# Kernel tuning notes

Measured on AMD Instinct MI355X. Metric: run time of the kernel, lower is better.

Reference implementation:

```python
import jax, jax.numpy as jnp
import numpy as np

N_NODES = 131072
N_EDGES = 4194304
H1, H2 = 16, 1


def setup_inputs() -> dict:
    key = jax.random.key(0)
    k = jax.random.split(key, 6)
    x = jax.random.uniform(k[0], (N_NODES, 2), dtype=jnp.float32)
    edge_index = jax.random.randint(k[1], (2, N_EDGES), 0, N_NODES, dtype=jnp.int64)
    # GCNConv weights (glorot-ish scale) and zero biases
    W1 = jax.random.normal(k[2], (2, H1), dtype=jnp.float32) * 0.5
    b1 = jnp.zeros((H1,), dtype=jnp.float32)
    W2 = jax.random.normal(k[3], (H1, H2), dtype=jnp.float32) * 0.25
    b2 = jnp.zeros((H2,), dtype=jnp.float32)
    return {"x": x, "W1": W1, "b1": b1, "W2": W2, "b2": b2, "edge_index": edge_index}


def gcn_layer(x, W, b, src, dst, n):
    # PyG GCNConv: h = D^{-1/2} (A+I) D^{-1/2} (x W) + b  (self-loops already in src/dst)
    h = x @ W                                              # [N, F_out]
    deg = jax.ops.segment_sum(jnp.ones(dst.shape[0], h.dtype), dst, num_segments=n)
    dinv = jax.lax.rsqrt(deg)                              # deg >= 1 thanks to self-loops
    norm = dinv[src] * dinv[dst]                           # [E+N]
    out = jax.ops.segment_sum(h[src] * norm[:, None], dst, num_segments=n)
    return out + b


def reference(x, W1, b1, W2, b2, edge_index):
    n = x.shape[0]
    loops = jnp.arange(n, dtype=edge_index.dtype)
    src = jnp.concatenate([edge_index[0], loops])          # add self-loops once
    dst = jnp.concatenate([edge_index[1], loops])
    h = jax.nn.relu(gcn_layer(x, W1, b1, src, dst, n))
    h = gcn_layer(h, W2, b2, src, dst, n)                  # [N, 1]
    scores = jax.nn.sigmoid(h)
    return scores[edge_index[0]]                           # gather per-edge source score [E, 1]
```

## Files before the change

### kernel.cpp

```cpp
#include <hip/hip_runtime.h>
#include <cmath>

typedef unsigned int uint;
typedef unsigned short u16;

constexpr int N  = 131072;
constexpr int E  = 4194304;
constexpr int F  = 16;
constexpr int NB = 512;
constexpr int NBLK  = 512;
constexpr int SCT   = 512;
constexpr int CHUNK = 8192;
constexpr int EPT   = 16;
constexpr int CAPB  = 9216;
constexpr int LT    = 1024;

constexpr float S1 = 4194304.0f;
constexpr float S2 = 65536.0f;

__global__ void __launch_bounds__(SCT) k_scatter(
        const int* __restrict__ src, const int* __restrict__ dst,
        uint* __restrict__ part, u16* __restrict__ cnt16, u16* __restrict__ dir16) {
    __shared__ uint h[NB];
    __shared__ uint wsum[8];
    __shared__ uint vals[CHUNK];
    int t = threadIdx.x, g = blockIdx.x;
    int lane = t & 63, w = t >> 6;
    h[t] = 0;
    __syncthreads();
    int d[EPT], s[EPT];
    const int4* src4 = (const int4*)src;
    const int4* dst4 = (const int4*)dst;
    int base4 = g * (CHUNK / 4);
#pragma unroll
    for (int k = 0; k < EPT / 4; ++k) {
        int4 d4 = dst4[base4 + k * SCT + t];
        int4 s4 = src4[base4 + k * SCT + t];
        d[4 * k + 0] = d4.x; d[4 * k + 1] = d4.y; d[4 * k + 2] = d4.z; d[4 * k + 3] = d4.w;
        s[4 * k + 0] = s4.x; s[4 * k + 1] = s4.y; s[4 * k + 2] = s4.z; s[4 * k + 3] = s4.w;
        atomicAdd(&h[d4.x >> 8], 1u);
        atomicAdd(&h[d4.y >> 8], 1u);
        atomicAdd(&h[d4.z >> 8], 1u);
        atomicAdd(&h[d4.w >> 8], 1u);
    }
    __syncthreads();
    uint v = h[t];
    uint sv = v;
#pragma unroll
    for (int off = 1; off < 64; off <<= 1) {
        uint n = __shfl_up(sv, off);
        if (lane >= off) sv += n;
    }
    if (lane == 63) wsum[w] = sv;
    __syncthreads();
    uint wo = 0;
    for (int i = 0; i < w; ++i) wo += wsum[i];
    sv += wo;
    uint ex = sv - v;
    cnt16[(size_t)t * NBLK + g] = (u16)v;
    dir16[(size_t)t * NBLK + g] = (u16)ex;
    __syncthreads();
    h[t] = ex;
    __syncthreads();
#pragma unroll
    for (int k = 0; k < EPT; ++k) {
        int b = d[k] >> 8;
        uint slot = atomicAdd(&h[b], 1u);
        vals[slot] = ((uint)s[k] << 8) | (uint)(d[k] & 255);
    }
    __syncthreads();
    uint4* part4 = (uint4*)(part + (size_t)g * CHUNK);
    const uint4* vals4 = (const uint4*)vals;
#pragma unroll
    for (int k = 0; k < EPT / 4; ++k)
        part4[k * SCT + t] = vals4[k * SCT + t];
}

__global__ void __launch_bounds__(SCT) k_gather(
        const uint* __restrict__ part, const u16* __restrict__ cnt16,
        const u16* __restrict__ dir16, const float* __restrict__ x,
        uint* __restrict__ part2, uint* __restrict__ blen,
        float* __restrict__ dinv, float2* __restrict__ y) {
    __shared__ uint ps[NB + 1];
    __shared__ uint segoff[NB];
    __shared__ uint hw[8 * 256];
    __shared__ uint wsum[8];
    __shared__ uint stage[CAPB];
    int t = threadIdx.x, b = blockIdx.x;
    int lane = t & 63, w = t >> 6;
#pragma unroll
    for (int k = 0; k < 4; ++k) hw[k * SCT + t] = 0;
    uint len = cnt16[(size_t)b * NBLK + t];
    segoff[t] = (uint)t * CHUNK + dir16[(size_t)b * NBLK + t];
    uint sv = len;
#pragma unroll
    for (int off = 1; off < 64; off <<= 1) {
        uint n = __shfl_up(sv, off);
        if (lane >= off) sv += n;
    }
    if (lane == 63) wsum[w] = sv;
    __syncthreads();
    uint wo = 0;
    for (int i = 0; i < w; ++i) wo += wsum[i];
    ps[t] = sv + wo - len;
    uint L = 0;
#pragma unroll
    for (int i = 0; i < 8; ++i) L += wsum[i];
    if (t == 0) ps[NB] = L;
    __syncthreads();
    for (uint i = t; i < L; i += SCT) {
        uint lo = 0, hi = NB;
        while (hi - lo > 1) {
            uint mid = (lo + hi) >> 1;
            if (ps[mid] <= i) lo = mid; else hi = mid;
        }
        uint pk = part[segoff[lo] + (i - ps[lo])];
        if (i < (uint)CAPB) stage[i] = pk;
        atomicAdd(&hw[w * 256 + (pk & 255u)], 1u);
    }
    __syncthreads();
    uint Lc = (L > (uint)CAPB) ? (uint)CAPB : L;
    uint* o2 = part2 + (size_t)b * CAPB;
    for (uint i = t; i < Lc; i += SCT) o2[i] = stage[i];
    if (t == 0) blen[b] = Lc;
    if (t < 256) {
        uint c = 0;
#pragma unroll
        for (int k = 0; k < 8; ++k) c += hw[k * 256 + t];
        int node = (b << 8) + t;
        float di = rsqrtf(1.0f + (float)c);
        dinv[node] = di;
        float2 xv = ((const float2*)x)[node];
        y[node] = make_float2(di * xv.x, di * xv.y);
    }
}

__global__ void __launch_bounds__(LT) k_l1(
        const uint* __restrict__ part2, const uint* __restrict__ blen,
        const float2* __restrict__ y, const float* __restrict__ dinv,
        const float* __restrict__ W1, const float* __restrict__ b1,
        const float* __restrict__ W2, float* __restrict__ g2) {
    __shared__ int a0[16 * 256], a1[16 * 256];
    int t = threadIdx.x, b = blockIdx.x, w = t >> 6;
#pragma unroll
    for (int k = 0; k < 4; ++k) { a0[k * LT + t] = 0; a1[k * LT + t] = 0; }
    __syncthreads();
    uint L = blen[b];
    const uint* p = part2 + (size_t)b * CAPB;
    for (uint i = t; i < L; i += LT) {
        uint pk = p[i];
        float2 ys = y[pk >> 8];
        atomicAdd(&a0[w * 256 + (pk & 255u)], __float2int_rn(ys.x * S1));
        atomicAdd(&a1[w * 256 + (pk & 255u)], __float2int_rn(ys.y * S1));
    }
    __syncthreads();
    if (t < 256) {
        int s0 = 0, s1 = 0;
#pragma unroll
        for (int k = 0; k < 16; ++k) { s0 += a0[k * 256 + t]; s1 += a1[k * 256 + t]; }
        int node = (b << 8) + t;
        float di = dinv[node];
        float2 yn = y[node];
        float A0 = di * ((float)s0 * (1.0f / S1) + yn.x);
        float A1 = di * ((float)s1 * (1.0f / S1) + yn.y);
        float acc = 0.0f;
#pragma unroll
        for (int f = 0; f < F; ++f) {
            float v = fmaf(A0, W1[f], fmaf(A1, W1[F + f], b1[f]));
            acc = fmaf(fmaxf(v, 0.0f), W2[f], acc);
        }
        g2[node] = di * acc;
    }
}

__global__ void __launch_bounds__(LT) k_l2(
        const uint* __restrict__ part2, const uint* __restrict__ blen,
        const float* __restrict__ g2, const float* __restrict__ dinv,
        const float* __restrict__ b2, float* __restrict__ scores) {
    __shared__ int a[16 * 256];
    int t = threadIdx.x, b = blockIdx.x, w = t >> 6;
#pragma unroll
    for (int k = 0; k < 4; ++k) a[k * LT + t] = 0;
    __syncthreads();
    uint L = blen[b];
    const uint* p = part2 + (size_t)b * CAPB;
    for (uint i = t; i < L; i += LT) {
        uint pk = p[i];
        atomicAdd(&a[w * 256 + (pk & 255u)], __float2int_rn(g2[pk >> 8] * S2));
    }
    __syncthreads();
    if (t < 256) {
        int s = 0;
#pragma unroll
        for (int k = 0; k < 16; ++k) s += a[k * 256 + t];
        int node = (b << 8) + t;
        float acc = (float)s * (1.0f / S2);
        float v = fmaf(dinv[node], acc + g2[node], b2[0]);
        scores[node] = 1.0f / (1.0f + expf(-v));
    }
}

__global__ void k_out(const int* __restrict__ src, const float* __restrict__ scores,
                      float* __restrict__ out) {
    int i = blockIdx.x * blockDim.x + threadIdx.x;
    if (i >= E / 4) return;
    int4 s4 = ((const int4*)src)[i];
    float4 o;
    o.x = scores[s4.x];
    o.y = scores[s4.y];
    o.z = scores[s4.z];
    o.w = scores[s4.w];
    ((float4*)out)[i] = o;
}

extern "C" void kernel_launch(void* const* d_in, const int* in_sizes, int n_in,
                              void* d_out, int out_size, void* d_ws, size_t ws_size,
                              hipStream_t stream) {
    const float* x  = (const float*)d_in[0];
    const float* W1 = (const float*)d_in[1];
    const float* b1 = (const float*)d_in[2];
    const float* W2 = (const float*)d_in[3];
    const float* b2 = (const float*)d_in[4];
    const int*   ei = (const int*)d_in[5];
    const int* src = ei;
    const int* dst = ei + E;

    u16* cnt16    = (u16*)d_ws;
    u16* dir16    = cnt16 + (size_t)NB * NBLK;
    uint* blen    = (uint*)(dir16 + (size_t)NB * NBLK);
    float* dinv   = (float*)(blen + NB);
    float2* y     = (float2*)(dinv + N);
    float* g2     = (float*)(y + N);
    float* scores = g2 + N;
    uint* part2   = (uint*)(scores + N);

    uint* part  = (uint*)d_out;
    float* out  = (float*)d_out;

    k_scatter<<<NBLK,        SCT, 0, stream>>>(src, dst, part, cnt16, dir16);
    k_gather <<<NB,          SCT, 0, stream>>>(part, cnt16, dir16, x, part2,
                                               blen, dinv, y);
    k_l1     <<<NB,          LT,  0, stream>>>(part2, blen, y, dinv, W1, b1, W2, g2);
    k_l2     <<<NB,          LT,  0, stream>>>(part2, blen, g2, dinv, b2, scores);
    k_out    <<<E / 4 / 256, 256, 0, stream>>>(src, scores, out);
}
```

Before: 176.3 us.

## Pack bucket directory, transpose it, widen gather blocks, vectorize partition reads

The scatter kernel now writes count and offset packed into one 32-bit word, stored coalesced in block-major order, and a new tiled transpose kernel reorders it for the gather kernel. This replaces the strided 16-bit directory stores. The gather kernel moves to 1024 threads and pads each bucket's partition with sentinel entries to a multiple of four. The two layer kernels can then read packed edges as uint4 and skip the sentinels. The cost is one extra kernel launch and a per-element sentinel branch in the hot loops.

Result: faster. 168.6 us, median of 2 (-4.4%).

```diff
diff --git a/kernel.cpp b/kernel.cpp
--- a/kernel.cpp
+++ b/kernel.cpp
@@ -2,7 +2,6 @@
 #include <cmath>
 
 typedef unsigned int uint;
-typedef unsigned short u16;
 
 constexpr int N  = 131072;
 constexpr int E  = 4194304;
@@ -10,17 +9,19 @@
 constexpr int NB = 512;
 constexpr int NBLK  = 512;
 constexpr int SCT   = 512;
+constexpr int GT    = 1024;
 constexpr int CHUNK = 8192;
 constexpr int EPT   = 16;
 constexpr int CAPB  = 9216;
 constexpr int LT    = 1024;
+constexpr uint SENT = 0xFFFFFFFFu;
 
 constexpr float S1 = 4194304.0f;
 constexpr float S2 = 65536.0f;
 
 __global__ void __launch_bounds__(SCT) k_scatter(
         const int* __restrict__ src, const int* __restrict__ dst,
-        uint* __restrict__ part, u16* __restrict__ cnt16, u16* __restrict__ dir16) {
+        uint* __restrict__ part, uint* __restrict__ dirw) {
     __shared__ uint h[NB];
     __shared__ uint wsum[8];
     __shared__ uint vals[CHUNK];
@@ -57,8 +58,7 @@
     for (int i = 0; i < w; ++i) wo += wsum[i];
     sv += wo;
     uint ex = sv - v;
-    cnt16[(size_t)t * NBLK + g] = (u16)v;
-    dir16[(size_t)t * NBLK + g] = (u16)ex;
+    dirw[(size_t)g * NB + t] = v | (ex << 16);
     __syncthreads();
     h[t] = ex;
     __syncthreads();
@@ -76,39 +76,57 @@
         part4[k * SCT + t] = vals4[k * SCT + t];
 }
 
-__global__ void __launch_bounds__(SCT) k_gather(
-        const uint* __restrict__ part, const u16* __restrict__ cnt16,
-        const u16* __restrict__ dir16, const float* __restrict__ x,
+__global__ void k_tr(const uint* __restrict__ in, uint* __restrict__ outm) {
+    __shared__ uint tile[32][33];
+    int bx = blockIdx.x, by = blockIdx.y;
+    int tx = threadIdx.x, ty = threadIdx.y;
+    tile[ty][tx] = in[(size_t)(by * 32 + ty) * NB + bx * 32 + tx];
+    __syncthreads();
+    outm[(size_t)(bx * 32 + ty) * NBLK + by * 32 + tx] = tile[tx][ty];
+}
+
+__global__ void __launch_bounds__(GT) k_gather(
+        const uint* __restrict__ part, const uint* __restrict__ dirT,
+        const float* __restrict__ x,
         uint* __restrict__ part2, uint* __restrict__ blen,
         float* __restrict__ dinv, float2* __restrict__ y) {
     __shared__ uint ps[NB + 1];
     __shared__ uint segoff[NB];
-    __shared__ uint hw[8 * 256];
+    __shared__ uint hw[16 * 256];
     __shared__ uint wsum[8];
     __shared__ uint stage[CAPB];
     int t = threadIdx.x, b = blockIdx.x;
     int lane = t & 63, w = t >> 6;
 #pragma unroll
-    for (int k = 0; k < 4; ++k) hw[k * SCT + t] = 0;
-    uint len = cnt16[(size_t)b * NBLK + t];
-    segoff[t] = (uint)t * CHUNK + dir16[(size_t)b * NBLK + t];
-    uint sv = len;
-#pragma unroll
-    for (int off = 1; off < 64; off <<= 1) {
-        uint n = __shfl_up(sv, off);
-        if (lane >= off) sv += n;
-    }
-    if (lane == 63) wsum[w] = sv;
-    __syncthreads();
-    uint wo = 0;
-    for (int i = 0; i < w; ++i) wo += wsum[i];
-    ps[t] = sv + wo - len;
-    uint L = 0;
-#pragma unroll
-    for (int i = 0; i < 8; ++i) L += wsum[i];
-    if (t == 0) ps[NB] = L;
-    __syncthreads();
-    for (uint i = t; i < L; i += SCT) {
+    for (int k = 0; k < 4; ++k) hw[k * GT + t] = 0;
+    if (t < NB) {
+        uint pd = dirT[(size_t)b * NBLK + t];
+        uint len = pd & 0xFFFFu;
+        segoff[t] = (uint)t * CHUNK + (pd >> 16);
+        uint sv = len;
+#pragma unroll
+        for (int off = 1; off < 64; off <<= 1) {
+            uint n = __shfl_up(sv, off);
+            if (lane >= off) sv += n;
+        }
+        if (lane == 63) wsum[w] = sv;
+        ps[t] = sv - len;
+    }
+    __syncthreads();
+    if (t < NB) {
+        uint wo = 0;
+        for (int i = 0; i < w; ++i) wo += wsum[i];
+        ps[t] += wo;
+    }
+    if (t == 0) {
+        uint L = 0;
+#pragma unroll
+        for (int i = 0; i < 8; ++i) L += wsum[i];
+        ps[NB] = L;
+    }
+    __syncthreads();
+    uint L = ps[NB];
+    for (uint i = t; i < L; i += GT) {
         uint lo = 0, hi = NB;
         while (hi - lo > 1) {
             uint mid = (lo + hi) >> 1;
@@ -120,13 +138,14 @@
     }
     __syncthreads();
     uint Lc = (L > (uint)CAPB) ? (uint)CAPB : L;
+    uint Lp = (Lc + 3u) & ~3u;
     uint* o2 = part2 + (size_t)b * CAPB;
-    for (uint i = t; i < Lc; i += SCT) o2[i] = stage[i];
-    if (t == 0) blen[b] = Lc;
+    for (uint i = t; i < Lp; i += GT) o2[i] = (i < Lc) ? stage[i] : SENT;
+    if (t == 0) blen[b] = Lp;
     if (t < 256) {
         uint c = 0;
 #pragma unroll
-        for (int k = 0; k < 8; ++k) c += hw[k * 256 + t];
+        for (int k = 0; k < 16; ++k) c += hw[k * 256 + t];
         int node = (b << 8) + t;
         float di = rsqrtf(1.0f + (float)c);
         dinv[node] = di;
@@ -145,13 +164,20 @@
 #pragma unroll
     for (int k = 0; k < 4; ++k) { a0[k * LT + t] = 0; a1[k * LT + t] = 0; }
     __syncthreads();
-    uint L = blen[b];
-    const uint* p = part2 + (size_t)b * CAPB;
-    for (uint i = t; i < L; i += LT) {
-        uint pk = p[i];
-        float2 ys = y[pk >> 8];
-        atomicAdd(&a0[w * 256 + (pk & 255u)], __float2int_rn(ys.x * S1));
-        atomicAdd(&a1[w * 256 + (pk & 255u)], __float2int_rn(ys.y * S1));
+    uint L4 = blen[b] >> 2;
+    const uint4* p4 = (const uint4*)(part2 + (size_t)b * CAPB);
+    for (uint i = t; i < L4; i += LT) {
+        uint4 q = p4[i];
+        uint pk;
+#pragma unroll
+        for (int k = 0; k < 4; ++k) {
+            pk = (k == 0) ? q.x : (k == 1) ? q.y : (k == 2) ? q.z : q.w;
+            if (pk != SENT) {
+                float2 ys = y[pk >> 8];
+                atomicAdd(&a0[w * 256 + (pk & 255u)], __float2int_rn(ys.x * S1));
+                atomicAdd(&a1[w * 256 + (pk & 255u)], __float2int_rn(ys.y * S1));
+            }
+        }
     }
     __syncthreads();
     if (t < 256) {
@@ -182,11 +208,17 @@
 #pragma unroll
     for (int k = 0; k < 4; ++k) a[k * LT + t] = 0;
     __syncthreads();
-    uint L = blen[b];
-    const uint* p = part2 + (size_t)b * CAPB;
-    for (uint i = t; i < L; i += LT) {
-        uint pk = p[i];
-        atomicAdd(&a[w * 256 + (pk & 255u)], __float2int_rn(g2[pk >> 8] * S2));
+    uint L4 = blen[b] >> 2;
+    const uint4* p4 = (const uint4*)(part2 + (size_t)b * CAPB);
+    for (uint i = t; i < L4; i += LT) {
+        uint4 q = p4[i];
+        uint pk;
+#pragma unroll
+        for (int k = 0; k < 4; ++k) {
+            pk = (k == 0) ? q.x : (k == 1) ? q.y : (k == 2) ? q.z : q.w;
+            if (pk != SENT)
+                atomicAdd(&a[w * 256 + (pk & 255u)], __float2int_rn(g2[pk >> 8] * S2));
+        }
     }
     __syncthreads();
     if (t < 256) {
@@ -225,9 +257,9 @@
     const int* src = ei;
     const int* dst = ei + E;
 
-    u16* cnt16    = (u16*)d_ws;
-    u16* dir16    = cnt16 + (size_t)NB * NBLK;
-    uint* blen    = (uint*)(dir16 + (size_t)NB * NBLK);
+    uint* dirw    = (uint*)d_ws;
+    uint* dirT    = dirw + (size_t)NBLK * NB;
+    uint* blen    = dirT + (size_t)NBLK * NB;
     float* dinv   = (float*)(blen + NB);
     float2* y     = (float2*)(dinv + N);
     float* g2     = (float*)(y + N);
@@ -237,10 +269,13 @@
     uint* part  = (uint*)d_out;
     float* out  = (float*)d_out;
 
-    k_scatter<<<NBLK,        SCT, 0, stream>>>(src, dst, part, cnt16, dir16);
-    k_gather <<<NB,          SCT, 0, stream>>>(part, cnt16, dir16, x, part2,
-                                               blen, dinv, y);
-    k_l1     <<<NB,          LT,  0, stream>>>(part2, blen, y, dinv, W1, b1, W2, g2);
-    k_l2     <<<NB,          LT,  0, stream>>>(part2, blen, g2, dinv, b2, scores);
-    k_out    <<<E / 4 / 256, 256, 0, stream>>>(src, scores, out);
-}
+    k_scatter<<<NBLK,              SCT,           0, stream>>>(src, dst, part, dirw);
+    k_tr     <<<dim3(16, 16),      dim3(32, 32),  0, stream>>>(dirw, dirT);
+    k_gather <<<NB,                GT,            0, stream>>>(part, dirT, x, part2,
+                                                               blen, dinv, y);
+    k_l1     <<<NB,                LT,            0, stream>>>(part2, blen, y, dinv,
+                                                               W1, b1, W2, g2);
+    k_l2     <<<NB,                LT,            0, stream>>>(part2, blen, g2, dinv,
+                                                               b2, scores);
+    k_out    <<<E / 4 / 256,       256,           0, stream>>>(src, scores, out);
+}
```
